# Performance work log

Measured on AMD Instinct MI355X. Metric: run time of the kernel, lower is better.

## Reference

```python
import jax, jax.numpy as jnp
import numpy as np

MIN_SCALE = 0.2
MAX_SCALE = 1.0
RESIDUAL_WEIGHT = 0.7


def _conv(x, w, b, pad):
    # x: [B,Cin,H,W], w: [Cout,Cin,k,k]
    y = jax.lax.conv_general_dilated(
        x, w, window_strides=(1, 1), padding=[(pad, pad), (pad, pad)],
        dimension_numbers=("NCHW", "OIHW", "NCHW"))
    return y + b[None, :, None, None]


def setup_inputs() -> dict:
    key = jax.random.key(0)
    ks = jax.random.split(key, 12)
    B, C, H, W = 16, 64, 256, 256
    hidden = C // 2  # max(1, in_channels // 2)
    s = lambda fan_in: 1.0 / np.sqrt(fan_in)
    return {
        "x": jax.random.normal(ks[0], (B, C, H, W), jnp.float32),
        # per-kernel spatial attention convs (2 -> 1 channels)
        "w3": jax.random.normal(ks[1], (1, 2, 3, 3), jnp.float32) * s(2 * 9),
        "b3": jnp.zeros((1,), jnp.float32),
        "w5": jax.random.normal(ks[2], (1, 2, 5, 5), jnp.float32) * s(2 * 25),
        "b5": jnp.zeros((1,), jnp.float32),
        # fusion conv (len(kernel_sizes)=2 -> 1 channels, 1x1)
        "wf": jax.random.normal(ks[3], (1, 2, 1, 1), jnp.float32) * s(2),
        "bf": jnp.zeros((1,), jnp.float32),
        # channel_reduction: C -> 1, 1x1
        "wr": jax.random.normal(ks[4], (1, C, 1, 1), jnp.float32) * s(C),
        "br": jnp.zeros((1,), jnp.float32),
        # channel_attention MLP: 1 -> hidden -> C (1x1 convs)
        "wc1": jax.random.normal(ks[5], (hidden, 1, 1, 1), jnp.float32),
        "bc1": jnp.zeros((hidden,), jnp.float32),
        "wc2": jax.random.normal(ks[6], (C, hidden, 1, 1), jnp.float32) * s(hidden),
        "bc2": jnp.zeros((C,), jnp.float32),
    }


def reference(x, w3, b3, w5, b5, wf, bf, wr, br, wc1, bc1, wc2, bc2):
    # channel-pooled descriptor, shared across scales: [B,2,H,W]
    x_cat = jnp.concatenate(
        [jnp.mean(x, axis=1, keepdims=True), jnp.max(x, axis=1, keepdims=True)],
        axis=1)
    a3 = jax.nn.sigmoid(_conv(x_cat, w3, b3, 1))  # [B,1,H,W]
    a5 = jax.nn.sigmoid(_conv(x_cat, w5, b5, 2))  # [B,1,H,W]
    fused = _conv(jnp.concatenate([a3, a5], axis=1), wf, bf, 0)  # [B,1,H,W]
    # dropout is identity at inference
    fused = MIN_SCALE + (MAX_SCALE - MIN_SCALE) * fused
    spatial = x * fused  # [B,C,H,W]
    # channel attention: reduce channels -> global avg pool -> 1x1 MLP -> sigmoid
    reduced = _conv(spatial, wr, br, 0)                         # [B,1,H,W]
    pooled = jnp.mean(reduced, axis=(2, 3), keepdims=True)      # [B,1,1,1]
    h = jax.nn.relu(_conv(pooled, wc1, bc1, 0))                 # [B,hid,1,1]
    cw = jax.nn.sigmoid(_conv(h, wc2, bc2, 0))                  # [B,C,1,1]
    spatial = spatial * cw
    return spatial + RESIDUAL_WEIGHT * x
```

## Files before the change

### kernel.cpp

```cpp
#include <hip/hip_runtime.h>
#include <math.h>

#define BATCH 16
#define CH 64
#define HH 256
#define WW 256
#define HW (HH*WW)
#define HW4 (HW/4)
#define HIDDEN 32

typedef float nfloat4 __attribute__((ext_vector_type(4)));

__global__ __launch_bounds__(256) void msa_k1_reduce(
    const float* __restrict__ x, const float* __restrict__ wr,
    float* __restrict__ mm, float* __restrict__ xrp)
{
    int idx = blockIdx.x * 256 + threadIdx.x;
    int b = idx / HW4;
    int p = idx % HW4;
    const float4* xb = (const float4*)x + (size_t)b * CH * HW4 + p;
    float sx = 0.f, sy = 0.f, sz = 0.f, sw = 0.f;
    float mx = -3.4e38f, my = -3.4e38f, mz = -3.4e38f, mw = -3.4e38f;
    float rx = 0.f, ry = 0.f, rz = 0.f, rw = 0.f;
    #pragma unroll 8
    for (int c = 0; c < CH; c++) {
        float4 v = xb[(size_t)c * HW4];
        float w = wr[c];
        sx += v.x; sy += v.y; sz += v.z; sw += v.w;
        mx = fmaxf(mx, v.x); my = fmaxf(my, v.y); mz = fmaxf(mz, v.z); mw = fmaxf(mw, v.w);
        rx += w * v.x; ry += w * v.y; rz += w * v.z; rw += w * v.w;
    }
    const float inv = 1.0f / CH;
    size_t o = (size_t)b * HW4 + p;
    float4 mm0 = {sx * inv, mx, sy * inv, my};
    float4 mm1 = {sz * inv, mz, sw * inv, mw};
    ((float4*)mm)[2 * o]     = mm0;
    ((float4*)mm)[2 * o + 1] = mm1;
    float4 xrv = {rx, ry, rz, rw};
    ((float4*)xrp)[o] = xrv;
}

__global__ __launch_bounds__(256) void msa_k2_conv(
    const float* __restrict__ mm, const float* __restrict__ xrp,
    const float* __restrict__ w3, const float* __restrict__ b3,
    const float* __restrict__ w5, const float* __restrict__ b5,
    const float* __restrict__ wf, const float* __restrict__ bf,
    float* __restrict__ fplane, float* __restrict__ sums)
{
    __shared__ float sm[2][20][20];
    __shared__ float red[256];
    int b = blockIdx.z;
    int h0 = blockIdx.y * 16, w0 = blockIdx.x * 16;
    int tx = threadIdx.x, ty = threadIdx.y;
    int tid = ty * 16 + tx;
    const float2* mb = (const float2*)mm + (size_t)b * HW;
    for (int l = tid; l < 400; l += 256) {
        int lh = l / 20, lw = l % 20;
        int gh = h0 + lh - 2, gw = w0 + lw - 2;
        float vm = 0.f, vx = 0.f;
        if (gh >= 0 && gh < HH && gw >= 0 && gw < WW) {
            float2 v = mb[gh * WW + gw];
            vm = v.x; vx = v.y;
        }
        sm[0][lh][lw] = vm;
        sm[1][lh][lw] = vx;
    }
    __syncthreads();
    float s3 = b3[0];
    #pragma unroll
    for (int kh = 0; kh < 3; kh++)
        #pragma unroll
        for (int kw = 0; kw < 3; kw++)
            s3 += sm[0][ty + 1 + kh][tx + 1 + kw] * w3[kh * 3 + kw]
                + sm[1][ty + 1 + kh][tx + 1 + kw] * w3[9 + kh * 3 + kw];
    float s5 = b5[0];
    #pragma unroll
    for (int kh = 0; kh < 5; kh++)
        #pragma unroll
        for (int kw = 0; kw < 5; kw++)
            s5 += sm[0][ty + kh][tx + kw] * w5[kh * 5 + kw]
                + sm[1][ty + kh][tx + kw] * w5[25 + kh * 5 + kw];
    float a3 = 1.f / (1.f + expf(-s3));
    float a5 = 1.f / (1.f + expf(-s5));
    float fused = wf[0] * a3 + wf[1] * a5 + bf[0];
    float f = 0.2f + 0.8f * fused;
    int gh = h0 + ty, gw = w0 + tx;
    size_t po = (size_t)b * HW + gh * WW + gw;
    fplane[po] = f;
    red[tid] = f * xrp[po];
    __syncthreads();
    for (int s = 128; s > 0; s >>= 1) {
        if (tid < s) red[tid] += red[tid + s];
        __syncthreads();
    }
    if (tid == 0) atomicAdd(&sums[b], red[0]);
}

__global__ void msa_k3_cw(
    const float* __restrict__ sums, const float* __restrict__ br,
    const float* __restrict__ wc1, const float* __restrict__ bc1,
    const float* __restrict__ wc2, const float* __restrict__ bc2,
    float* __restrict__ cw)
{
    __shared__ float hsh[HIDDEN];
    int b = blockIdx.x;
    int t = threadIdx.x;
    float pooled = sums[b] * (1.0f / HW) + br[0];
    if (t < HIDDEN) hsh[t] = fmaxf(wc1[t] * pooled + bc1[t], 0.f);
    __syncthreads();
    if (t < CH) {
        float acc = bc2[t];
        #pragma unroll
        for (int j = 0; j < HIDDEN; j++) acc += wc2[t * HIDDEN + j] * hsh[j];
        cw[b * CH + t] = 1.f / (1.f + expf(-acc));
    }
}

__global__ __launch_bounds__(256) void msa_k4_out(
    const float* __restrict__ x, const float* __restrict__ fplane,
    const float* __restrict__ cw, float* __restrict__ out)
{
    int bi = gridDim.x - 1 - blockIdx.x;
    int idx = bi * 256 + threadIdx.x;
    int p = idx & (HW4 - 1);
    int bc = idx >> 14;
    int b = bc >> 6;
    float s = cw[bc];
    float4 xv = ((const float4*)x)[idx];
    float4 fv = ((const float4*)fplane)[(size_t)b * HW4 + p];
    nfloat4 o;
    o.x = xv.x * (fv.x * s + 0.7f);
    o.y = xv.y * (fv.y * s + 0.7f);
    o.z = xv.z * (fv.z * s + 0.7f);
    o.w = xv.w * (fv.w * s + 0.7f);
    __builtin_nontemporal_store(o, ((nfloat4*)out) + idx);
}

extern "C" void kernel_launch(void* const* d_in, const int* in_sizes, int n_in,
                              void* d_out, int out_size, void* d_ws, size_t ws_size,
                              hipStream_t stream) {
    const float* x   = (const float*)d_in[0];
    const float* w3  = (const float*)d_in[1];
    const float* b3  = (const float*)d_in[2];
    const float* w5  = (const float*)d_in[3];
    const float* b5  = (const float*)d_in[4];
    const float* wf  = (const float*)d_in[5];
    const float* bf  = (const float*)d_in[6];
    const float* wr  = (const float*)d_in[7];
    const float* br  = (const float*)d_in[8];
    const float* wc1 = (const float*)d_in[9];
    const float* bc1 = (const float*)d_in[10];
    const float* wc2 = (const float*)d_in[11];
    const float* bc2 = (const float*)d_in[12];

    float* ws    = (float*)d_ws;
    float* mm    = ws;
    float* xrp   = ws + (size_t)2 * BATCH * HW;
    float* fpl   = ws + (size_t)3 * BATCH * HW;
    float* sums  = ws + (size_t)4 * BATCH * HW;
    float* cw    = sums + BATCH;

    (void)hipMemsetAsync(sums, 0, BATCH * sizeof(float), stream);

    msa_k1_reduce<<<BATCH * HW4 / 256, 256, 0, stream>>>(x, wr, mm, xrp);

    dim3 g2(WW / 16, HH / 16, BATCH);
    msa_k2_conv<<<g2, dim3(16, 16), 0, stream>>>(mm, xrp, w3, b3, w5, b5,
                                                 wf, bf, fpl, sums);

    msa_k3_cw<<<BATCH, 64, 0, stream>>>(sums, br, wc1, bc1, wc2, bc2, cw);

    msa_k4_out<<<BATCH * CH * HW4 / 256, 256, 0, stream>>>(x, fpl, cw, (float*)d_out);
}
```

Measured before the change: 564.3 us.

## Process batch in groups so x stays cache-resident between reduce and output

Splits the batch into groups of four and runs the reduce, conv and output kernels per group, so the x slice read by the reduce pass may still sit in the large last-level cache when the output pass reads it again. The channel-attention MLP is folded into the conv kernel via a last-block-done atomic counter, which removes one launch. The reduce kernel now splits channels across four waves with a shared-memory combine to raise parallelism, and the block reduction uses wave shuffles. In exchange there are many more small launches, with tail effects between groups.

```diff
diff --git a/kernel.cpp b/kernel.cpp
--- a/kernel.cpp
+++ b/kernel.cpp
@@ -8,36 +8,62 @@
 #define HW (HH*WW)
 #define HW4 (HW/4)
 #define HIDDEN 32
+#define GRP 4
+#define NGRP (BATCH/GRP)
+#define K2_BPB 256
 
 typedef float nfloat4 __attribute__((ext_vector_type(4)));
 
 __global__ __launch_bounds__(256) void msa_k1_reduce(
     const float* __restrict__ x, const float* __restrict__ wr,
-    float* __restrict__ mm, float* __restrict__ xrp)
+    float* __restrict__ mm, float* __restrict__ xrp, int b0)
 {
-    int idx = blockIdx.x * 256 + threadIdx.x;
-    int b = idx / HW4;
-    int p = idx % HW4;
-    const float4* xb = (const float4*)x + (size_t)b * CH * HW4 + p;
+    __shared__ float part[3][64][13];
+    int t = threadIdx.x;
+    int p = t & 63;
+    int q = t >> 6;
+    int i4 = blockIdx.x * 64 + p;
+    int bl = i4 >> 14;
+    int p4 = i4 & (HW4 - 1);
+    int b = b0 + bl;
+    const float4* xb = (const float4*)x + (size_t)(b * CH + q * 16) * HW4 + p4;
     float sx = 0.f, sy = 0.f, sz = 0.f, sw = 0.f;
     float mx = -3.4e38f, my = -3.4e38f, mz = -3.4e38f, mw = -3.4e38f;
     float rx = 0.f, ry = 0.f, rz = 0.f, rw = 0.f;
-    #pragma unroll 8
-    for (int c = 0; c < CH; c++) {
+    #pragma unroll 16
+    for (int c = 0; c < 16; c++) {
         float4 v = xb[(size_t)c * HW4];
-        float w = wr[c];
+        float w = wr[q * 16 + c];
         sx += v.x; sy += v.y; sz += v.z; sw += v.w;
-        mx = fmaxf(mx, v.x); my = fmaxf(my, v.y); mz = fmaxf(mz, v.z); mw = fmaxf(mw, v.w);
+        mx = fmaxf(mx, v.x); my = fmaxf(my, v.y);
+        mz = fmaxf(mz, v.z); mw = fmaxf(mw, v.w);
         rx += w * v.x; ry += w * v.y; rz += w * v.z; rw += w * v.w;
     }
-    const float inv = 1.0f / CH;
-    size_t o = (size_t)b * HW4 + p;
-    float4 mm0 = {sx * inv, mx, sy * inv, my};
-    float4 mm1 = {sz * inv, mz, sw * inv, mw};
-    ((float4*)mm)[2 * o]     = mm0;
-    ((float4*)mm)[2 * o + 1] = mm1;
-    float4 xrv = {rx, ry, rz, rw};
-    ((float4*)xrp)[o] = xrv;
+    if (q) {
+        float* d = part[q - 1][p];
+        d[0] = sx; d[1] = sy; d[2] = sz; d[3] = sw;
+        d[4] = mx; d[5] = my; d[6] = mz; d[7] = mw;
+        d[8] = rx; d[9] = ry; d[10] = rz; d[11] = rw;
+    }
+    __syncthreads();
+    if (q == 0) {
+        #pragma unroll
+        for (int k = 0; k < 3; k++) {
+            const float* d = part[k][p];
+            sx += d[0]; sy += d[1]; sz += d[2]; sw += d[3];
+            mx = fmaxf(mx, d[4]); my = fmaxf(my, d[5]);
+            mz = fmaxf(mz, d[6]); mw = fmaxf(mw, d[7]);
+            rx += d[8]; ry += d[9]; rz += d[10]; rw += d[11];
+        }
+        const float inv = 1.0f / CH;
+        size_t o = (size_t)b * HW4 + p4;
+        float4 mm0 = {sx * inv, mx, sy * inv, my};
+        float4 mm1 = {sz * inv, mz, sw * inv, mw};
+        ((float4*)mm)[2 * o]     = mm0;
+        ((float4*)mm)[2 * o + 1] = mm1;
+        float4 xrv = {rx, ry, rz, rw};
+        ((float4*)xrp)[o] = xrv;
+    }
 }
 
 __global__ __launch_bounds__(256) void msa_k2_conv(
@@ -45,11 +71,18 @@
     const float* __restrict__ w3, const float* __restrict__ b3,
     const float* __restrict__ w5, const float* __restrict__ b5,
     const float* __restrict__ wf, const float* __restrict__ bf,
-    float* __restrict__ fplane, float* __restrict__ sums)
+    const float* __restrict__ br,
+    const float* __restrict__ wc1, const float* __restrict__ bc1,
+    const float* __restrict__ wc2, const float* __restrict__ bc2,
+    float* __restrict__ fplane, float* __restrict__ sums,
+    unsigned* __restrict__ cnt, float* __restrict__ cw, int b0)
 {
     __shared__ float sm[2][20][20];
-    __shared__ float red[256];
-    int b = blockIdx.z;
+    __shared__ float wsum[4];
+    __shared__ int lastflag;
+    __shared__ float pooledS;
+    __shared__ float hsh[HIDDEN];
+    int b = b0 + blockIdx.z;
     int h0 = blockIdx.y * 16, w0 = blockIdx.x * 16;
     int tx = threadIdx.x, ty = threadIdx.y;
     int tid = ty * 16 + tx;
@@ -87,53 +120,55 @@
     int gh = h0 + ty, gw = w0 + tx;
     size_t po = (size_t)b * HW + gh * WW + gw;
     fplane[po] = f;
-    red[tid] = f * xrp[po];
-    __syncthreads();
-    for (int s = 128; s > 0; s >>= 1) {
-        if (tid < s) red[tid] += red[tid + s];
+    float v = f * xrp[po];
+    #pragma unroll
+    for (int off = 32; off > 0; off >>= 1) v += __shfl_down(v, off);
+    if ((tid & 63) == 0) wsum[tid >> 6] = v;
+    __syncthreads();
+    if (tid == 0) {
+        float tot = wsum[0] + wsum[1] + wsum[2] + wsum[3];
+        atomicAdd(&sums[b], tot);
+        __threadfence();
+        unsigned old = atomicAdd(&cnt[b], 1u);
+        lastflag = (old == K2_BPB - 1) ? 1 : 0;
+    }
+    __syncthreads();
+    if (lastflag) {
+        if (tid == 0) {
+            float tot = atomicAdd(&sums[b], 0.0f);
+            pooledS = tot * (1.0f / HW) + br[0];
+        }
         __syncthreads();
-    }
-    if (tid == 0) atomicAdd(&sums[b], red[0]);
-}
-
-__global__ void msa_k3_cw(
-    const float* __restrict__ sums, const float* __restrict__ br,
-    const float* __restrict__ wc1, const float* __restrict__ bc1,
-    const float* __restrict__ wc2, const float* __restrict__ bc2,
-    float* __restrict__ cw)
-{
-    __shared__ float hsh[HIDDEN];
-    int b = blockIdx.x;
-    int t = threadIdx.x;
-    float pooled = sums[b] * (1.0f / HW) + br[0];
-    if (t < HIDDEN) hsh[t] = fmaxf(wc1[t] * pooled + bc1[t], 0.f);
-    __syncthreads();
-    if (t < CH) {
-        float acc = bc2[t];
-        #pragma unroll
-        for (int j = 0; j < HIDDEN; j++) acc += wc2[t * HIDDEN + j] * hsh[j];
-        cw[b * CH + t] = 1.f / (1.f + expf(-acc));
+        if (tid < HIDDEN) hsh[tid] = fmaxf(wc1[tid] * pooledS + bc1[tid], 0.f);
+        __syncthreads();
+        if (tid < CH) {
+            float acc = bc2[tid];
+            #pragma unroll
+            for (int j = 0; j < HIDDEN; j++) acc += wc2[tid * HIDDEN + j] * hsh[j];
+            cw[b * CH + tid] = 1.f / (1.f + expf(-acc));
+        }
     }
 }
 
 __global__ __launch_bounds__(256) void msa_k4_out(
     const float* __restrict__ x, const float* __restrict__ fplane,
-    const float* __restrict__ cw, float* __restrict__ out)
+    const float* __restrict__ cw, float* __restrict__ out, int b0)
 {
-    int bi = gridDim.x - 1 - blockIdx.x;
-    int idx = bi * 256 + threadIdx.x;
+    int idx = blockIdx.x * 256 + threadIdx.x;
+    size_t base = (size_t)b0 * CH * HW4;
     int p = idx & (HW4 - 1);
     int bc = idx >> 14;
-    int b = bc >> 6;
-    float s = cw[bc];
-    float4 xv = ((const float4*)x)[idx];
+    int bl = bc >> 6;
+    int b = b0 + bl;
+    float s = cw[b * CH + (bc & 63)];
+    float4 xv = ((const float4*)x)[base + idx];
     float4 fv = ((const float4*)fplane)[(size_t)b * HW4 + p];
     nfloat4 o;
     o.x = xv.x * (fv.x * s + 0.7f);
     o.y = xv.y * (fv.y * s + 0.7f);
     o.z = xv.z * (fv.z * s + 0.7f);
     o.w = xv.w * (fv.w * s + 0.7f);
-    __builtin_nontemporal_store(o, ((nfloat4*)out) + idx);
+    __builtin_nontemporal_store(o, ((nfloat4*)out) + base + idx);
 }
 
 extern "C" void kernel_launch(void* const* d_in, const int* in_sizes, int n_in,
@@ -158,17 +193,19 @@
     float* xrp   = ws + (size_t)2 * BATCH * HW;
     float* fpl   = ws + (size_t)3 * BATCH * HW;
     float* sums  = ws + (size_t)4 * BATCH * HW;
-    float* cw    = sums + BATCH;
-
-    (void)hipMemsetAsync(sums, 0, BATCH * sizeof(float), stream);
-
-    msa_k1_reduce<<<BATCH * HW4 / 256, 256, 0, stream>>>(x, wr, mm, xrp);
-
-    dim3 g2(WW / 16, HH / 16, BATCH);
-    msa_k2_conv<<<g2, dim3(16, 16), 0, stream>>>(mm, xrp, w3, b3, w5, b5,
-                                                 wf, bf, fpl, sums);
-
-    msa_k3_cw<<<BATCH, 64, 0, stream>>>(sums, br, wc1, bc1, wc2, bc2, cw);
-
-    msa_k4_out<<<BATCH * CH * HW4 / 256, 256, 0, stream>>>(x, fpl, cw, (float*)d_out);
-}
+    unsigned* cnt = (unsigned*)(sums + BATCH);
+    float* cw    = sums + 2 * BATCH;
+
+    (void)hipMemsetAsync(sums, 0, 2 * BATCH * sizeof(float), stream);
+
+    for (int g = 0; g < NGRP; ++g) {
+        int b0 = g * GRP;
+        msa_k1_reduce<<<GRP * HW4 / 64, 256, 0, stream>>>(x, wr, mm, xrp, b0);
+        dim3 g2(WW / 16, HH / 16, GRP);
+        msa_k2_conv<<<g2, dim3(16, 16), 0, stream>>>(mm, xrp, w3, b3, w5, b5,
+                                                     wf, bf, br, wc1, bc1, wc2, bc2,
+                                                     fpl, sums, cnt, cw, b0);
+        msa_k4_out<<<GRP * CH * HW4 / 256, 256, 0, stream>>>(x, fpl, cw,
+                                                             (float*)d_out, b0);
+    }
+}
```

After: 620.1 us. 1.1x slower.
